# Optimization experiments

Measured on AMD Instinct MI355X. Metric: run time of the kernel, lower is better.

## Reference

```python
import jax, jax.numpy as jnp
import numpy as np

N = 100000
E = 1600000
IN_DIM, HID_DIM, OUT_DIM = 128, 64, 32
HEADS = 8
NEG_SLOPE = 0.2
NEG_INF = -1e9


def _glorot(key, shape):
    stdv = np.sqrt(6.0 / (shape[-2] + shape[-1]))
    return jax.random.uniform(key, shape, jnp.float32, -stdv, stdv)


def gat_conv(x, src, dst, self_mask, W, att, bias, heads, out_ch, concat):
    """One GATConv layer (eval mode: dropout off). src/dst already include self-loops;
    self_mask marks original edges that were self-loops (removed via -inf score)."""
    n = x.shape[0]
    h = (x @ W).reshape(n, heads, out_ch)              # [N,H,C]
    x_i = h[dst]                                        # [Etot,H,C] gather target
    x_j = h[src]                                        # [Etot,H,C] gather source
    a = jnp.einsum('ehc,hc->eh', x_i, att[0, :, :out_ch]) \
        + jnp.einsum('ehc,hc->eh', x_j, att[0, :, out_ch:])
    alpha = jax.nn.leaky_relu(a, NEG_SLOPE)             # [Etot,H]
    alpha = jnp.where(self_mask[:, None], NEG_INF, alpha)
    amax = jax.lax.stop_gradient(
        jax.ops.segment_max(alpha, dst, num_segments=n))
    ex = jnp.exp(alpha - amax[dst])
    denom = jax.ops.segment_sum(ex, dst, num_segments=n)
    w = ex / denom[dst]                                 # segment softmax over incoming edges
    out = jax.ops.segment_sum(x_j * w[:, :, None], dst, num_segments=n)  # [N,H,C]
    out = out.reshape(n, heads * out_ch) if concat else out.mean(axis=1)
    return out + bias


def setup_inputs() -> dict:
    key = jax.random.key(0)
    ks = jax.random.split(key, 12)
    x = jax.random.normal(ks[0], (N, IN_DIM), jnp.float32)
    edge_index = jax.random.randint(ks[1], (2, E), 0, N, jnp.int64)
    c1 = HID_DIM // HEADS  # 8
    params = {
        'W1': _glorot(ks[2], (IN_DIM, HEADS * c1)),
        'att1': _glorot(ks[3], (1, HEADS, 2 * c1)),
        'b1': jnp.zeros((HID_DIM,), jnp.float32),
        'W2': _glorot(ks[4], (HID_DIM, HEADS * c1)),
        'att2': _glorot(ks[5], (1, HEADS, 2 * c1)),
        'b2': jnp.zeros((HID_DIM,), jnp.float32),
        'W3': _glorot(ks[6], (HID_DIM, 1 * OUT_DIM)),
        'att3': _glorot(ks[7], (1, 1, 2 * OUT_DIM)),
        'b3': jnp.zeros((OUT_DIM,), jnp.float32),
    }
    return dict(x=x, edge_index=edge_index, **params)


def reference(x, edge_index, W1, att1, b1, W2, att2, b2, W3, att3, b3):
    n = x.shape[0]
    src, dst = edge_index[0], edge_index[1]
    loop = jnp.arange(n, dtype=src.dtype)
    src_f = jnp.concatenate([src, loop])
    dst_f = jnp.concatenate([dst, loop])
    # remove_self_loops + add_self_loops: mask original self-loops, append fresh ones
    self_mask = jnp.concatenate([src == dst, jnp.zeros((n,), bool)])
    c1 = HID_DIM // HEADS
    h = jax.nn.elu(gat_conv(x, src_f, dst_f, self_mask, W1, att1, b1, HEADS, c1, True))
    h = jax.nn.elu(gat_conv(h, src_f, dst_f, self_mask, W2, att2, b2, HEADS, c1, True))
    out = gat_conv(h, src_f, dst_f, self_mask, W3, att3, b3, 1, OUT_DIM, False)
    return out
```

## Files before the change

### kernel.cpp

```cpp
#include <hip/hip_runtime.h>
#include <hip/hip_bf16.h>

#define NN 100000
#define EE 1600000

constexpr int SCAN_BLK = 1024;
constexpr int NB_SCAN  = (NN + SCAN_BLK - 1) / SCAN_BLK;

constexpr int NR  = 8;
constexpr int RS  = NN / NR;
constexpr int CB  = 200;
constexpr int CE  = EE / CB;


__global__ void zero_int(int* __restrict__ p, int n) {
    int i = blockIdx.x * 256 + threadIdx.x;
    if (i < n) p[i] = 0;
}

__global__ __launch_bounds__(256) void hist_rank_k(const int* __restrict__ ei,
                                                   int* __restrict__ deg,
                                                   int* __restrict__ rank) {
    int base = blockIdx.x * 1024;
    const int* __restrict__ dstp = ei + EE;
    int tid = threadIdx.x;
    int d[4], s[4], r[4];
    #pragma unroll
    for (int k = 0; k < 4; ++k) {
        int off = base + tid + k * 256;
        bool v = off < EE;
        d[k] = v ? dstp[off] : -1;
        s[k] = v ? ei[off]   : -1;
        r[k] = 0;
    }
    #pragma unroll
    for (int k = 0; k < 4; ++k) {
        if (d[k] >= 0 && s[k] != d[k]) r[k] = atomicAdd(&deg[d[k]], 1);
    }
    #pragma unroll
    for (int k = 0; k < 4; ++k) {
        int off = base + tid + k * 256;
        if (off < EE) rank[off] = r[k];
    }
}

__global__ void sum_blocks(const int* __restrict__ deg, int* __restrict__ partials) {
    __shared__ int sh[256];
    int t = threadIdx.x;
    int base = blockIdx.x * SCAN_BLK + t * 4;
    int s = 0;
    #pragma unroll
    for (int k = 0; k < 4; ++k) { int i = base + k; if (i < NN) s += deg[i]; }
    sh[t] = s; __syncthreads();
    for (int off = 128; off > 0; off >>= 1) {
        if (t < off) sh[t] += sh[t + off];
        __syncthreads();
    }
    if (t == 0) partials[blockIdx.x] = sh[0];
}

__global__ void scan_partials(int* __restrict__ partials) {
    __shared__ int sh[128];
    int t = threadIdx.x;
    int v = (t < NB_SCAN) ? partials[t] : 0;
    sh[t] = v;
    __syncthreads();
    for (int off = 1; off < 128; off <<= 1) {
        int tmp = (t >= off) ? sh[t - off] : 0;
        __syncthreads();
        sh[t] += tmp;
        __syncthreads();
    }
    if (t < NB_SCAN) partials[t] = sh[t] - v;
}

__global__ void scan_final(const int* __restrict__ deg, const int* __restrict__ partials,
                           int* __restrict__ rowptr) {
    __shared__ int sh[256];
    int t = threadIdx.x;
    int base = blockIdx.x * SCAN_BLK + t * 4;
    int v[4]; int s = 0;
    #pragma unroll
    for (int k = 0; k < 4; ++k) { int i = base + k; v[k] = (i < NN) ? deg[i] : 0; s += v[k]; }
    sh[t] = s; __syncthreads();
    for (int off = 1; off < 256; off <<= 1) {
        int tmp = (t >= off) ? sh[t - off] : 0;
        __syncthreads();
        sh[t] += tmp;
        __syncthreads();
    }
    int pref = partials[blockIdx.x] + sh[t] - s;
    #pragma unroll
    for (int k = 0; k < 4; ++k) {
        int i = base + k;
        if (i < NN) {
            rowptr[i] = pref; pref += v[k];
            if (i == NN - 1) rowptr[NN] = pref;
        }
    }
}

__global__ __launch_bounds__(256) void scatter2_k(const int* __restrict__ ei,
                                                  const int* __restrict__ rank,
                                                  const int* __restrict__ rowptr,
                                                  int* __restrict__ col) {
    int rg = blockIdx.x % NR, chunk = blockIdx.x / NR;
    int lo = rg * RS, hi = lo + RS;
    const int* __restrict__ dstp = ei + EE;
    int base = chunk * CE;
    int tid = threadIdx.x;
    for (int ii = 0; ii < CE; ii += 1024) {
        int d[4], s[4], rk[4];
        #pragma unroll
        for (int k = 0; k < 4; ++k) {
            int off = ii + tid + k * 256;
            int i = base + off;
            bool v = off < CE;
            d[k]  = v ? dstp[i] : -1;
            s[k]  = v ? ei[i]   : -1;
            rk[k] = v ? rank[i] : 0;
        }
        int p[4]; bool keep[4];
        #pragma unroll
        for (int k = 0; k < 4; ++k) {
            keep[k] = (d[k] >= lo && d[k] < hi && s[k] != d[k]);
            if (keep[k]) p[k] = rowptr[d[k]] + rk[k];
        }
        #pragma unroll
        for (int k = 0; k < 4; ++k) {
            if (keep[k]) col[p[k]] = s[k];
        }
    }
}


template<int K, int M, int H, int NPB, int RSU>
__global__ __launch_bounds__(256) void gemm_tile(const float* __restrict__ xin,
                          const float* __restrict__ W,
                          const float* __restrict__ att,
                          unsigned* __restrict__ Rb,
                          float* __restrict__ sdst) {
    constexpr int C   = M / H;
    constexpr int MG  = M / 4;
    constexpr int NG  = NPB / 4;
    static_assert(MG * NG == 256, "tile mismatch");
    constexpr int K4  = K / 4;
    constexpr int KC4 = (K4 > 16) ? 16 : K4;
    constexpr int NCH = K4 / KC4;

    __shared__ float4 Wq[K * MG];
    __shared__ float4 Xq[NPB * KC4];

    int tid = threadIdx.x;
    const float4* W4 = (const float4*)W;
    for (int i = tid; i < K * MG; i += 256) Wq[i] = W4[i];

    int node0 = blockIdx.x * NPB;
    const float4* x4 = (const float4*)xin;

    int mg = tid % MG, ng = tid / MG;
    int nb = ng * 4;
    float acc[4][4];
    #pragma unroll
    for (int i = 0; i < 4; ++i)
        #pragma unroll
        for (int j = 0; j < 4; ++j) acc[i][j] = 0.f;

    for (int ch = 0; ch < NCH; ++ch) {
        __syncthreads();
        for (int i = tid; i < NPB * KC4; i += 256) {
            int n = i / KC4, k4l = i % KC4;
            int node = node0 + n;
            float4 v = make_float4(0.f, 0.f, 0.f, 0.f);
            if (node < NN) v = x4[(size_t)node * K4 + ch * KC4 + k4l];
            Xq[i] = v;
        }
        __syncthreads();
        #pragma unroll 4
        for (int k4 = 0; k4 < KC4; ++k4) {
            float4 xv[4], wv[4];
            #pragma unroll
            for (int i = 0; i < 4; ++i) xv[i] = Xq[(nb + i) * KC4 + k4];
            int kbase = (ch * KC4 + k4) * 4;
            #pragma unroll
            for (int kk = 0; kk < 4; ++kk) wv[kk] = Wq[(kbase + kk) * MG + mg];
            #pragma unroll
            for (int i = 0; i < 4; ++i) {
                const float* xf = (const float*)&xv[i];
                #pragma unroll
                for (int kk = 0; kk < 4; ++kk) {
                    const float* wf = (const float*)&wv[kk];
                    float xs = xf[kk];
                    acc[i][0] = fmaf(xs, wf[0], acc[i][0]);
                    acc[i][1] = fmaf(xs, wf[1], acc[i][1]);
                    acc[i][2] = fmaf(xs, wf[2], acc[i][2]);
                    acc[i][3] = fmaf(xs, wf[3], acc[i][3]);
                }
            }
        }
    }

    constexpr int TPH = C / 4;
    int head = mg / TPH;
    int c0   = (mg % TPH) * 4;
    float ad[4], as_[4];
    #pragma unroll
    for (int j = 0; j < 4; ++j) {
        ad[j]  = att[head * 2 * C + c0 + j];
        as_[j] = att[head * 2 * C + C + c0 + j];
    }
    #pragma unroll
    for (int i = 0; i < 4; ++i) {
        int node = node0 + nb + i;
        if (node < NN) {
            unsigned short us[4];
            #pragma unroll
            for (int j = 0; j < 4; ++j) {
                __hip_bfloat16 b = __float2bfloat16(acc[i][j]);
                us[j] = *(unsigned short*)&b;
            }
            uint2 pk;
            pk.x = (unsigned)us[0] | ((unsigned)us[1] << 16);
            pk.y = (unsigned)us[2] | ((unsigned)us[3] << 16);
            *(uint2*)(Rb + (size_t)node * RSU + 8 + 2 * mg) = pk;
        }
        float pd = acc[i][0]*ad[0]  + acc[i][1]*ad[1]  + acc[i][2]*ad[2]  + acc[i][3]*ad[3];
        float ps = acc[i][0]*as_[0] + acc[i][1]*as_[1] + acc[i][2]*as_[2] + acc[i][3]*as_[3];
        #pragma unroll
        for (int off = 1; off < TPH; off <<= 1) {
            pd += __shfl_xor(pd, off, 64);
            ps += __shfl_xor(ps, off, 64);
        }
        if ((mg % TPH) == 0 && node < NN) {
            sdst[node * H + head] = pd;
            ((float*)(Rb + (size_t)node * RSU))[head] = ps;
        }
    }
}


template<int CT, int H, int U, int RSU, bool ELU_OUT>
__global__ __launch_bounds__(256) void agg_k(const int* __restrict__ rowptr, const int* __restrict__ col,
                      const float* __restrict__ sdst, const unsigned* __restrict__ Rb,
                      const float* __restrict__ bias, float* __restrict__ output) {
    constexpr int C    = CT / H;
    constexpr int CP   = CT / 2;
    constexpr int G    = 64 / CP;
    constexpr int NL   = U / G;
    constexpr int EPEL = (U * H >= 64) ? (U * H) / 64 : 1;
    static_assert(EPEL == 1 || EPEL == 2, "mapping");

    int lane = threadIdx.x & 63;
    int node = blockIdx.x * (blockDim.x >> 6) + (threadIdx.x >> 6);
    if (node >= NN) return;

    int cp = lane % CP;
    int pp = lane / CP;
    int hh = (2 * cp) / C;
    int eh = lane % H;
    int gb = lane / H;

    float sd = (lane < U * H) ? sdst[node * H + eh] : 0.f;

    int start = rowptr[node], end = rowptr[node + 1];
    int total = end + 1;
    float2 acc = make_float2(0.f, 0.f);
    float dsum = 0.f;

    for (int j = start; j < total; j += U) {
        int cv = node;
        {
            int idx = j + lane;
            if (lane < U && idx < end) cv = col[idx];
        }
        float e1 = 0.f, e2 = 0.f;
        if (EPEL == 2) {
            int b1 = __shfl(cv, gb, 64);
            int b2 = __shfl(cv, gb + U / 2, 64);
            float s1 = ((const float*)(Rb + (size_t)b1 * RSU))[eh];
            float s2 = ((const float*)(Rb + (size_t)b2 * RSU))[eh];
            float a1 = sd + s1; a1 = (a1 >= 0.f) ? a1 : 0.2f * a1;
            float a2 = sd + s2; a2 = (a2 >= 0.f) ? a2 : 0.2f * a2;
            if (j + gb < total)          e1 = __expf(a1);
            if (j + gb + U / 2 < total)  e2 = __expf(a2);
            dsum += e1 + e2;
        } else {
            if (lane < U * H) {
                float s1 = ((const float*)(Rb + (size_t)cv * RSU))[eh];
                float a1 = sd + s1; a1 = (a1 >= 0.f) ? a1 : 0.2f * a1;
                if (j + gb < total) e1 = __expf(a1);
                dsum += e1;
            }
        }
        unsigned hv[NL];
        #pragma unroll
        for (int t = 0; t < NL; ++t) {
            int se = __shfl(cv, t * G + pp, 64);
            hv[t] = Rb[(size_t)se * RSU + 8 + cp];
        }
        #pragma unroll
        for (int t = 0; t < NL; ++t) {
            int eidx = t * G + pp;
            float ex;
            if (EPEL == 2)
                ex = __shfl((t < NL / 2) ? e1 : e2, (eidx & (U / 2 - 1)) * H + hh, 64);
            else
                ex = __shfl(e1, eidx * H + hh, 64);
            float hx = __uint_as_float(hv[t] << 16);
            float hy = __uint_as_float(hv[t] & 0xffff0000u);
            acc.x = fmaf(ex, hx, acc.x);
            acc.y = fmaf(ex, hy, acc.y);
        }
    }
    #pragma unroll
    for (int off = H; off < 64; off <<= 1) dsum += __shfl_xor(dsum, off, 64);
    float den = __shfl(dsum, hh, 64);
    #pragma unroll
    for (int off = CP; off < 64; off <<= 1) {
        acc.x += __shfl_xor(acc.x, off, 64);
        acc.y += __shfl_xor(acc.y, off, 64);
    }
    if (lane < CP) {
        float inv = 1.f / den;
        float vx = acc.x * inv + bias[2 * cp];
        float vy = acc.y * inv + bias[2 * cp + 1];
        if (ELU_OUT) {
            vx = (vx > 0.f) ? vx : expm1f(vx);
            vy = (vy > 0.f) ? vy : expm1f(vy);
        }
        ((float2*)output)[(size_t)node * CP + cp] = make_float2(vx, vy);
    }
}


extern "C" void kernel_launch(void* const* d_in, const int* in_sizes, int n_in,
                              void* d_out, int out_size, void* d_ws, size_t ws_size,
                              hipStream_t stream) {
    const float* x    = (const float*)d_in[0];
    const int*   ei   = (const int*)d_in[1];
    const float* W1   = (const float*)d_in[2];
    const float* att1 = (const float*)d_in[3];
    const float* b1   = (const float*)d_in[4];
    const float* W2   = (const float*)d_in[5];
    const float* att2 = (const float*)d_in[6];
    const float* b2   = (const float*)d_in[7];
    const float* W3   = (const float*)d_in[8];
    const float* att3 = (const float*)d_in[9];
    const float* b3   = (const float*)d_in[10];
    float* out = (float*)d_out;

    char* p = (char*)d_ws;
    auto alloc = [&](size_t bytes) -> void* {
        void* r = (void*)p;
        p += (bytes + 255) & ~(size_t)255;
        return r;
    };
    int*   rowptr   = (int*)alloc((NN + 1) * sizeof(int));
    int*   deg      = (int*)alloc(NN * sizeof(int));
    int*   partials = (int*)alloc(NB_SCAN * sizeof(int));
    int*   col      = (int*)alloc(EE * sizeof(int));
    int*   rank     = (int*)alloc(EE * sizeof(int));
    float* sdst     = (float*)alloc((size_t)NN * 8 * sizeof(float));
    unsigned* Rb    = (unsigned*)alloc((size_t)NN * 48 * sizeof(unsigned));
    float* Fb       = (float*)alloc((size_t)NN * 64 * sizeof(float));

    zero_int<<<(NN + 255) / 256, 256, 0, stream>>>(deg, NN);
    hist_rank_k<<<(EE + 1023) / 1024, 256, 0, stream>>>(ei, deg, rank);
    sum_blocks<<<NB_SCAN, 256, 0, stream>>>(deg, partials);
    scan_partials<<<1, 128, 0, stream>>>(partials);
    scan_final<<<NB_SCAN, 256, 0, stream>>>(deg, partials, rowptr);
    scatter2_k<<<CB * NR, 256, 0, stream>>>(ei, rank, rowptr, col);

    gemm_tile<128, 64, 8, 64, 48><<<(NN + 63) / 64, 256, 0, stream>>>(x, W1, att1, Rb, sdst);
    agg_k<64, 8, 16, 48, true><<<(NN + 3) / 4, 256, 0, stream>>>(rowptr, col, sdst, Rb, b1, Fb);

    gemm_tile<64, 64, 8, 64, 48><<<(NN + 63) / 64, 256, 0, stream>>>(Fb, W2, att2, Rb, sdst);
    agg_k<64, 8, 16, 48, true><<<(NN + 3) / 4, 256, 0, stream>>>(rowptr, col, sdst, Rb, b2, Fb);

    gemm_tile<64, 32, 1, 128, 32><<<(NN + 127) / 128, 256, 0, stream>>>(Fb, W3, att3, Rb, sdst);
    agg_k<32, 1, 32, 32, false><<<(NN + 3) / 4, 256, 0, stream>>>(rowptr, col, sdst, Rb, b3, out);
}
```

Measured before the change: 450.0 us.

## Replicate degree counters to spread histogram atomics across copies

The degree histogram now goes into eight replicated counter arrays, with each block choosing a replica by block index. This spreads atomic contention and L2 hot-spotting across the copies. A combine kernel turns the replicas into per-replica exclusive offsets plus a total degree. scan_final adds the row prefix into every replica, so scatter can compute edge positions from its replica's offset. Work per block also doubles (2048 edges, 8 per thread), at the cost of extra memory traffic over the 8×N arrays and one extra kernel launch.

```diff
diff --git a/kernel.cpp b/kernel.cpp
--- a/kernel.cpp
+++ b/kernel.cpp
@@ -11,6 +11,8 @@
 constexpr int RS  = NN / NR;
 constexpr int CB  = 200;
 constexpr int CE  = EE / CB;
+constexpr int RPL = 8;
+constexpr int HB  = 2048;
 
 
 __global__ void zero_int(int* __restrict__ p, int n) {
@@ -19,14 +21,15 @@
 }
 
 __global__ __launch_bounds__(256) void hist_rank_k(const int* __restrict__ ei,
-                                                   int* __restrict__ deg,
+                                                   int* __restrict__ degR,
                                                    int* __restrict__ rank) {
-    int base = blockIdx.x * 1024;
+    int base = blockIdx.x * HB;
+    int* __restrict__ deg = degR + (size_t)(blockIdx.x & (RPL - 1)) * NN;
     const int* __restrict__ dstp = ei + EE;
     int tid = threadIdx.x;
-    int d[4], s[4], r[4];
-    #pragma unroll
-    for (int k = 0; k < 4; ++k) {
+    int d[8], s[8], r[8];
+    #pragma unroll
+    for (int k = 0; k < 8; ++k) {
         int off = base + tid + k * 256;
         bool v = off < EE;
         d[k] = v ? dstp[off] : -1;
@@ -34,13 +37,27 @@
         r[k] = 0;
     }
     #pragma unroll
-    for (int k = 0; k < 4; ++k) {
+    for (int k = 0; k < 8; ++k) {
         if (d[k] >= 0 && s[k] != d[k]) r[k] = atomicAdd(&deg[d[k]], 1);
     }
     #pragma unroll
-    for (int k = 0; k < 4; ++k) {
+    for (int k = 0; k < 8; ++k) {
         int off = base + tid + k * 256;
         if (off < EE) rank[off] = r[k];
+    }
+}
+
+__global__ void combine_k(int* __restrict__ degR, int* __restrict__ deg) {
+    int d = blockIdx.x * 256 + threadIdx.x;
+    if (d < NN) {
+        int run = 0;
+        #pragma unroll
+        for (int r = 0; r < RPL; ++r) {
+            int v = degR[(size_t)r * NN + d];
+            degR[(size_t)r * NN + d] = run;
+            run += v;
+        }
+        deg[d] = run;
     }
 }
 
@@ -75,7 +92,7 @@
 }
 
 __global__ void scan_final(const int* __restrict__ deg, const int* __restrict__ partials,
-                           int* __restrict__ rowptr) {
+                           int* __restrict__ rowptr, int* __restrict__ degR) {
     __shared__ int sh[256];
     int t = threadIdx.x;
     int base = blockIdx.x * SCAN_BLK + t * 4;
@@ -94,7 +111,10 @@
     for (int k = 0; k < 4; ++k) {
         int i = base + k;
         if (i < NN) {
-            rowptr[i] = pref; pref += v[k];
+            rowptr[i] = pref;
+            #pragma unroll
+            for (int r = 0; r < RPL; ++r) degR[(size_t)r * NN + i] += pref;
+            pref += v[k];
             if (i == NN - 1) rowptr[NN] = pref;
         }
     }
@@ -102,32 +122,36 @@
 
 __global__ __launch_bounds__(256) void scatter2_k(const int* __restrict__ ei,
                                                   const int* __restrict__ rank,
-                                                  const int* __restrict__ rowptr,
+                                                  const int* __restrict__ degR,
                                                   int* __restrict__ col) {
     int rg = blockIdx.x % NR, chunk = blockIdx.x / NR;
     int lo = rg * RS, hi = lo + RS;
     const int* __restrict__ dstp = ei + EE;
     int base = chunk * CE;
     int tid = threadIdx.x;
-    for (int ii = 0; ii < CE; ii += 1024) {
-        int d[4], s[4], rk[4];
-        #pragma unroll
-        for (int k = 0; k < 4; ++k) {
+    for (int ii = 0; ii < CE; ii += 2048) {
+        int d[8], s[8], rk[8], ix[8];
+        #pragma unroll
+        for (int k = 0; k < 8; ++k) {
             int off = ii + tid + k * 256;
             int i = base + off;
             bool v = off < CE;
+            ix[k] = i;
             d[k]  = v ? dstp[i] : -1;
             s[k]  = v ? ei[i]   : -1;
             rk[k] = v ? rank[i] : 0;
         }
-        int p[4]; bool keep[4];
-        #pragma unroll
-        for (int k = 0; k < 4; ++k) {
+        int p[8]; bool keep[8];
+        #pragma unroll
+        for (int k = 0; k < 8; ++k) {
             keep[k] = (d[k] >= lo && d[k] < hi && s[k] != d[k]);
-            if (keep[k]) p[k] = rowptr[d[k]] + rk[k];
-        }
-        #pragma unroll
-        for (int k = 0; k < 4; ++k) {
+            if (keep[k]) {
+                int rep = (ix[k] / HB) & (RPL - 1);
+                p[k] = degR[(size_t)rep * NN + d[k]] + rk[k];
+            }
+        }
+        #pragma unroll
+        for (int k = 0; k < 8; ++k) {
             if (keep[k]) col[p[k]] = s[k];
         }
     }
@@ -357,6 +381,7 @@
     };
     int*   rowptr   = (int*)alloc((NN + 1) * sizeof(int));
     int*   deg      = (int*)alloc(NN * sizeof(int));
+    int*   degR     = (int*)alloc((size_t)RPL * NN * sizeof(int));
     int*   partials = (int*)alloc(NB_SCAN * sizeof(int));
     int*   col      = (int*)alloc(EE * sizeof(int));
     int*   rank     = (int*)alloc(EE * sizeof(int));
@@ -364,12 +389,13 @@
     unsigned* Rb    = (unsigned*)alloc((size_t)NN * 48 * sizeof(unsigned));
     float* Fb       = (float*)alloc((size_t)NN * 64 * sizeof(float));
 
-    zero_int<<<(NN + 255) / 256, 256, 0, stream>>>(deg, NN);
-    hist_rank_k<<<(EE + 1023) / 1024, 256, 0, stream>>>(ei, deg, rank);
+    zero_int<<<(RPL * NN + 255) / 256, 256, 0, stream>>>(degR, RPL * NN);
+    hist_rank_k<<<(EE + HB - 1) / HB, 256, 0, stream>>>(ei, degR, rank);
+    combine_k<<<(NN + 255) / 256, 256, 0, stream>>>(degR, deg);
     sum_blocks<<<NB_SCAN, 256, 0, stream>>>(deg, partials);
     scan_partials<<<1, 128, 0, stream>>>(partials);
-    scan_final<<<NB_SCAN, 256, 0, stream>>>(deg, partials, rowptr);
-    scatter2_k<<<CB * NR, 256, 0, stream>>>(ei, rank, rowptr, col);
+    scan_final<<<NB_SCAN, 256, 0, stream>>>(deg, partials, rowptr, degR);
+    scatter2_k<<<CB * NR, 256, 0, stream>>>(ei, rank, degR, col);
 
     gemm_tile<128, 64, 8, 64, 48><<<(NN + 63) / 64, 256, 0, stream>>>(x, W1, att1, Rb, sdst);
     agg_k<64, 8, 16, 48, true><<<(NN + 3) / 4, 256, 0, stream>>>(rowptr, col, sdst, Rb, b1, Fb);
```

Measured after the change: 461.4 us. 1.03x slower.
